# Kernel tuning notes

Measured on AMD Instinct MI355X. Metric: run time of the kernel, lower is better.

The kernel has to match this reference:

```python
import jax, jax.numpy as jnp
import numpy as np

# Static config (mirrors FBPinn __init__ args)
NW = 16            # nwindows (1D case)
D0, D1 = 0.0, 100.0  # domain
OVERLAP = 0.25
SIGMA = 0.5
HIDDEN = 3         # number of hidden layers in each subdomain NN
NEURONS = 64
U_MEAN, U_SD = 0.0, 1.0
N = 100_000        # number of collocation points


def _geometry():
    """partition_domain + get_midpoints + get_midpoints_overlap (1D)."""
    width = (D1 - D0) / NW
    i = np.arange(NW)
    lo = np.where(i == 0, D0, D0 + (i - OVERLAP / 2) * width)
    hi = np.where(i == NW - 1, D1, D0 + (i + 1 + OVERLAP / 2) * width)
    means = (lo + hi) / 2
    std = (hi - lo) / 2
    ovm = np.empty(NW + 1)
    ovm[0] = lo[0]
    ovm[NW] = hi[-1]
    ovm[1:NW] = (hi[:-1] + lo[1:]) / 2  # midpoint of each overlap region
    f32 = lambda a: jnp.asarray(a, jnp.float32)
    return f32(lo), f32(hi), f32(means), f32(std), f32(ovm)


def setup_inputs() -> dict:
    key = jax.random.key(0)
    ks = jax.random.split(key, 7)
    x = jax.random.uniform(ks[0], (N,), jnp.float32, minval=D0, maxval=D1)
    s_in = 1.0  # fan_in = 1
    s_h = 1.0 / np.sqrt(NEURONS)
    return {
        "x": x,
        "W_in": jax.random.normal(ks[1], (NW, NEURONS), jnp.float32) * s_in,
        "b_in": jax.random.normal(ks[2], (NW, NEURONS), jnp.float32) * 0.1,
        "W_h": jax.random.normal(ks[3], (HIDDEN - 1, NW, NEURONS, NEURONS), jnp.float32) * s_h,
        "b_h": jax.random.normal(ks[4], (HIDDEN - 1, NW, NEURONS), jnp.float32) * 0.1,
        "W_out": jax.random.normal(ks[5], (NW, NEURONS), jnp.float32) * s_h,
        "b_out": jax.random.normal(ks[6], (NW,), jnp.float32) * 0.1,
    }


def reference(x, W_in, b_in, W_h, b_h, W_out, b_out):
    lo, hi, means, std, ovm = _geometry()
    # Normalize inputs per subdomain: [W, N]
    xn = (x[None, :] - means[:, None]) / std[:, None]
    # Batched per-window MLP (tanh), one fused pass over all windows.
    h = jnp.tanh(xn[:, :, None] * W_in[:, None, :] + b_in[:, None, :])  # [W, N, H]
    for l in range(HIDDEN - 1):
        h = jnp.tanh(jnp.einsum("wni,wio->wno", h, W_h[l]) + b_h[l][:, None, :])
    out = jnp.einsum("wni,wi->wn", h, W_out) + b_out[:, None]  # [W, N]
    out = out * U_SD + U_MEAN
    # Sigmoid window functions (compute_window, 1D): [W, N]
    win = jax.nn.sigmoid((x[None, :] - ovm[:-1, None]) / SIGMA) * \
          jax.nn.sigmoid(-(x[None, :] - ovm[1:, None]) / SIGMA)
    # Strict in-subdomain mask, as in forward(): (lo < x) & (x < hi)
    mask = (lo[:, None] < x[None, :]) & (x[None, :] < hi[:, None])
    pred = jnp.sum(jnp.where(mask, win * out, jnp.float32(0.0)), axis=0)  # [N]
    return pred
```

## Files before the change

kernel.cpp:

```cpp
#include <hip/hip_runtime.h>


#define NW    16
#define NEUR  64
#define BLK   256
#define CAP   10240
#define CSTR  16
#define GX    64
#define DSFENCE() asm volatile("" ::: "memory")

typedef _Float16 v8h __attribute__((ext_vector_type(8)));
typedef float    v4f __attribute__((ext_vector_type(4)));
typedef _Float16 h2  __attribute__((ext_vector_type(2)));
typedef unsigned v4u __attribute__((ext_vector_type(4)));

__device__ __forceinline__ float fast_tanh(float x) {
    float e = __expf(x + x);
    return 1.0f - 2.0f * __builtin_amdgcn_rcpf(e + 1.0f);
}
__device__ __forceinline__ float fast_sigmoid(float z) {
    return __builtin_amdgcn_rcpf(1.0f + __expf(-z));
}
__device__ __forceinline__ v8h zero8() {
    v8h z;
    #pragma unroll
    for (int j = 0; j < 8; ++j) z[j] = (_Float16)0.0f;
    return z;
}

__global__ __launch_bounds__(1024) void pass1_bucket(
    const float* __restrict__ x, int n,
    int* __restrict__ cnt, int* __restrict__ list,
    float* __restrict__ out) {
    __shared__ int lcnt[NW];
    __shared__ int lbase[NW];
    const int tid = threadIdx.x;
    if (tid < NW) lcnt[tid] = 0;
    __syncthreads();

    const int i = blockIdx.x * 1024 + tid;
    int w0 = -1, w1 = -1, p0 = 0, p1 = 0;
    if (i < n) {
        out[i] = 0.0f;
        float xv = x[i];
        #pragma unroll
        for (int w = 0; w < NW; ++w) {
            float lo = (w == 0)      ? 0.0f   : ((float)w - 0.125f) * 6.25f;
            float hi = (w == NW - 1) ? 100.0f : ((float)w + 1.125f) * 6.25f;
            if (lo < xv && xv < hi) {
                if (w0 < 0) w0 = w; else w1 = w;
            }
        }
        if (w0 >= 0) p0 = atomicAdd(&lcnt[w0], 1);
        if (w1 >= 0) p1 = atomicAdd(&lcnt[w1], 1);
    }
    __syncthreads();
    if (tid < NW)
        lbase[tid] = atomicAdd(&cnt[tid * CSTR], lcnt[tid]);
    __syncthreads();

    if (w0 >= 0) { int p = lbase[w0] + p0; if (p < CAP) list[w0 * CAP + p] = i; }
    if (w1 >= 0) { int p = lbase[w1] + p1; if (p < CAP) list[w1 * CAP + p] = i; }
}

__global__ __launch_bounds__(256) void pass2_mlp(
    const float* __restrict__ x,
    const float* __restrict__ W_in, const float* __restrict__ b_in,
    const float* __restrict__ W_h,  const float* __restrict__ b_h,
    const float* __restrict__ W_out, const float* __restrict__ b_out,
    const int* __restrict__ cnt, const int* __restrict__ list,
    float* __restrict__ out, int npts) {
    __shared__ _Float16 aH[16 * 512];
    __shared__ _Float16 aIn[4 * 512];
    __shared__ _Float16 aOut[2 * 512];
    __shared__ float    biasH[128];
    __shared__ unsigned Hp[4 * 1024];

    const int tid = threadIdx.x;
    const int w   = blockIdx.y;
    const int count = min(cnt[w * CSTR], GX * 128);
    if (blockIdx.x * 128 >= count) return;

    const int lane = tid & 63;
    const int wid  = tid >> 6;
    const int n16  = lane & 15;
    const int quad = lane >> 4;

    #pragma unroll
    for (int p = 0; p < 4; ++p) {
        int f  = wid * 4 + p;
        int l  = f >> 3, mt = (f >> 1) & 3, ks = f & 1;
        const float* Ws = W_h + (l * NW + w) * 4096;
        int m  = mt * 16 + n16;
        int k0 = ks * 32 + quad * 8;
        v8h a;
        #pragma unroll
        for (int j = 0; j < 8; ++j)
            a[j] = (_Float16)Ws[(k0 + j) * 64 + m];
        *(v8h*)(&aH[f * 512 + lane * 8]) = a;
    }
    {
        int mt = wid, m = mt * 16 + n16;
        v8h a = zero8();
        if (quad == 0) {
            a[0] = (_Float16)W_in[w * 64 + m];
            a[1] = (_Float16)b_in[w * 64 + m];
        }
        *(v8h*)(&aIn[mt * 512 + lane * 8]) = a;
    }
    if (wid < 2) {
        int ks = wid;
        v8h a = zero8();
        if (n16 == 0) {
            int k0 = ks * 32 + quad * 8;
            #pragma unroll
            for (int j = 0; j < 8; ++j)
                a[j] = (_Float16)W_out[w * 64 + k0 + j];
        }
        *(v8h*)(&aOut[ks * 512 + lane * 8]) = a;
    }
    if (tid < 128)
        biasH[tid] = b_h[((tid >> 6) * NW + w) * 64 + (tid & 63)];
    __syncthreads();

    float lo = (w == 0)      ? 0.0f   : ((float)w - 0.125f) * 6.25f;
    float hi = (w == NW - 1) ? 100.0f : ((float)w + 1.125f) * 6.25f;
    float mean    = 0.5f * (lo + hi);
    float inv_std = 1.0f / (0.5f * (hi - lo));
    float ow0 = (float)w * 6.25f;
    float ow1 = (float)(w + 1) * 6.25f;
    float bo  = b_out[w];

    float xv[2], xn[2];
    bool  act[2];
    int   idx[2];
    #pragma unroll
    for (int t = 0; t < 2; ++t) {
        int kpt = blockIdx.x * 128 + wid * 32 + t * 16 + n16;
        act[t]  = (kpt < count) && (lane < 16);
        int kk  = (kpt < count) ? kpt : 0;
        int id  = list[w * CAP + kk];
        if ((unsigned)id >= (unsigned)npts) id = 0;
        idx[t] = id;
        xv[t]  = x[id];
        xn[t]  = (xv[t] - mean) * inv_std;
    }

    unsigned* HpW = Hp + wid * 1024;

    {
        v8h b[2];
        #pragma unroll
        for (int t = 0; t < 2; ++t) {
            b[t] = zero8();
            if (quad == 0) { b[t][0] = (_Float16)xn[t]; b[t][1] = (_Float16)1.0f; }
        }
        #pragma unroll
        for (int mt = 0; mt < 4; ++mt) {
            v8h a = *(const v8h*)(&aIn[mt * 512 + lane * 8]);
            #pragma unroll
            for (int t = 0; t < 2; ++t) {
                v4f c = {0.0f, 0.0f, 0.0f, 0.0f};
                c = __builtin_amdgcn_mfma_f32_16x16x32_f16(a, b[t], c, 0, 0, 0);
                int k2 = mt * 8 + quad * 2;
                h2 q0, q1;
                q0[0] = (_Float16)fast_tanh(c[0]);
                q0[1] = (_Float16)fast_tanh(c[1]);
                q1[0] = (_Float16)fast_tanh(c[2]);
                q1[1] = (_Float16)fast_tanh(c[3]);
                HpW[t * 512 + k2 * 16 + n16]       = __builtin_bit_cast(unsigned, q0);
                HpW[t * 512 + (k2 + 1) * 16 + n16] = __builtin_bit_cast(unsigned, q1);
            }
        }
    }
    DSFENCE();

    #pragma unroll
    for (int l = 0; l < 2; ++l) {
        v4f d[2][4];
        #pragma unroll
        for (int t = 0; t < 2; ++t)
            #pragma unroll
            for (int mt = 0; mt < 4; ++mt)
                d[t][mt] = (v4f){0.0f, 0.0f, 0.0f, 0.0f};
        #pragma unroll
        for (int ks = 0; ks < 2; ++ks) {
            v8h b[2];
            #pragma unroll
            for (int t = 0; t < 2; ++t) {
                v4u bw;
                #pragma unroll
                for (int j2 = 0; j2 < 4; ++j2)
                    bw[j2] = HpW[t * 512 + (ks * 16 + quad * 4 + j2) * 16 + n16];
                b[t] = __builtin_bit_cast(v8h, bw);
            }
            #pragma unroll
            for (int mt = 0; mt < 4; ++mt) {
                v8h a = *(const v8h*)(&aH[(l * 8 + mt * 2 + ks) * 512 + lane * 8]);
                #pragma unroll
                for (int t = 0; t < 2; ++t)
                    d[t][mt] = __builtin_amdgcn_mfma_f32_16x16x32_f16(
                                   a, b[t], d[t][mt], 0, 0, 0);
            }
        }
        DSFENCE();
        const float* bl = biasH + l * 64;
        #pragma unroll
        for (int t = 0; t < 2; ++t) {
            #pragma unroll
            for (int mt = 0; mt < 4; ++mt) {
                int m0 = mt * 16 + quad * 4;
                int k2 = m0 >> 1;
                h2 q0, q1;
                q0[0] = (_Float16)fast_tanh(d[t][mt][0] + bl[m0]);
                q0[1] = (_Float16)fast_tanh(d[t][mt][1] + bl[m0 + 1]);
                q1[0] = (_Float16)fast_tanh(d[t][mt][2] + bl[m0 + 2]);
                q1[1] = (_Float16)fast_tanh(d[t][mt][3] + bl[m0 + 3]);
                HpW[t * 512 + k2 * 16 + n16]       = __builtin_bit_cast(unsigned, q0);
                HpW[t * 512 + (k2 + 1) * 16 + n16] = __builtin_bit_cast(unsigned, q1);
            }
        }
        DSFENCE();
    }

    {
        v4f e[2] = {{0.0f,0.0f,0.0f,0.0f}, {0.0f,0.0f,0.0f,0.0f}};
        #pragma unroll
        for (int ks = 0; ks < 2; ++ks) {
            v8h a = *(const v8h*)(&aOut[ks * 512 + lane * 8]);
            #pragma unroll
            for (int t = 0; t < 2; ++t) {
                v4u bw;
                #pragma unroll
                for (int j2 = 0; j2 < 4; ++j2)
                    bw[j2] = HpW[t * 512 + (ks * 16 + quad * 4 + j2) * 16 + n16];
                v8h b = __builtin_bit_cast(v8h, bw);
                e[t] = __builtin_amdgcn_mfma_f32_16x16x32_f16(a, b, e[t], 0, 0, 0);
            }
        }
        #pragma unroll
        for (int t = 0; t < 2; ++t) {
            float outv = e[t][0] + bo;
            float win = fast_sigmoid((xv[t] - ow0) * 2.0f) *
                        fast_sigmoid((ow1 - xv[t]) * 2.0f);
            if (act[t]) atomicAdd(&out[idx[t]], win * outv);
        }
    }
}

extern "C" void kernel_launch(void* const* d_in, const int* in_sizes, int n_in,
                              void* d_out, int out_size, void* d_ws, size_t ws_size,
                              hipStream_t stream) {
    const float* x     = (const float*)d_in[0];
    const float* W_in  = (const float*)d_in[1];
    const float* b_in  = (const float*)d_in[2];
    const float* W_h   = (const float*)d_in[3];
    const float* b_h   = (const float*)d_in[4];
    const float* W_out = (const float*)d_in[5];
    const float* b_out = (const float*)d_in[6];
    float* out = (float*)d_out;
    const int n = in_sizes[0];

    int* cnt  = (int*)d_ws;
    int* list = (int*)((char*)d_ws + 1024);

    hipMemsetAsync(cnt, 0, NW * CSTR * sizeof(int), stream);

    pass1_bucket<<<(n + 1023) / 1024, 1024, 0, stream>>>(x, n, cnt, list, out);

    dim3 grid(GX, NW);
    pass2_mlp<<<grid, BLK, 0, stream>>>(x, W_in, b_in, W_h, b_h, W_out, b_out,
                                        cnt, list, out, n);
}
```

Before: 85.66 us.

## Fuse bucketing into MLP kernel with per-block shared-memory point lists

Replaces the global bucketing pass and its workspace list with a single kernel. Each (segment, window) block scans its 1/64 slice of x, collects in-window points into a shared-memory index list, then loops over them in 128-point tiles through the MFMA MLP. Output zeroing moves to a memset. This removes one kernel launch, the global atomics and the list round-trip through global memory. In exchange, every block reads its whole x segment for all 16 windows, and LCAP=1600 relies on the uniform input distribution to avoid overflowing the shared list.

```diff
diff --git a/kernel.cpp b/kernel.cpp
--- a/kernel.cpp
+++ b/kernel.cpp
@@ -4,9 +4,8 @@
 #define NW    16
 #define NEUR  64
 #define BLK   256
-#define CAP   10240
-#define CSTR  16
-#define GX    64
+#define NSEG  64
+#define LCAP  1600
 #define DSFENCE() asm volatile("" ::: "memory")
 
 typedef _Float16 v8h __attribute__((ext_vector_type(8)));
@@ -28,63 +27,45 @@
     return z;
 }
 
-__global__ __launch_bounds__(1024) void pass1_bucket(
-    const float* __restrict__ x, int n,
-    int* __restrict__ cnt, int* __restrict__ list,
-    float* __restrict__ out) {
-    __shared__ int lcnt[NW];
-    __shared__ int lbase[NW];
-    const int tid = threadIdx.x;
-    if (tid < NW) lcnt[tid] = 0;
-    __syncthreads();
-
-    const int i = blockIdx.x * 1024 + tid;
-    int w0 = -1, w1 = -1, p0 = 0, p1 = 0;
-    if (i < n) {
-        out[i] = 0.0f;
-        float xv = x[i];
-        #pragma unroll
-        for (int w = 0; w < NW; ++w) {
-            float lo = (w == 0)      ? 0.0f   : ((float)w - 0.125f) * 6.25f;
-            float hi = (w == NW - 1) ? 100.0f : ((float)w + 1.125f) * 6.25f;
-            if (lo < xv && xv < hi) {
-                if (w0 < 0) w0 = w; else w1 = w;
-            }
-        }
-        if (w0 >= 0) p0 = atomicAdd(&lcnt[w0], 1);
-        if (w1 >= 0) p1 = atomicAdd(&lcnt[w1], 1);
-    }
-    __syncthreads();
-    if (tid < NW)
-        lbase[tid] = atomicAdd(&cnt[tid * CSTR], lcnt[tid]);
-    __syncthreads();
-
-    if (w0 >= 0) { int p = lbase[w0] + p0; if (p < CAP) list[w0 * CAP + p] = i; }
-    if (w1 >= 0) { int p = lbase[w1] + p1; if (p < CAP) list[w1 * CAP + p] = i; }
-}
-
-__global__ __launch_bounds__(256) void pass2_mlp(
+__global__ __launch_bounds__(256, 3) void fused_fbpinn(
     const float* __restrict__ x,
     const float* __restrict__ W_in, const float* __restrict__ b_in,
     const float* __restrict__ W_h,  const float* __restrict__ b_h,
     const float* __restrict__ W_out, const float* __restrict__ b_out,
-    const int* __restrict__ cnt, const int* __restrict__ list,
-    float* __restrict__ out, int npts) {
+    float* __restrict__ out, int n) {
     __shared__ _Float16 aH[16 * 512];
     __shared__ _Float16 aIn[4 * 512];
     __shared__ _Float16 aOut[2 * 512];
     __shared__ float    biasH[128];
     __shared__ unsigned Hp[4 * 1024];
-
-    const int tid = threadIdx.x;
-    const int w   = blockIdx.y;
-    const int count = min(cnt[w * CSTR], GX * 128);
-    if (blockIdx.x * 128 >= count) return;
-
+    __shared__ int      lidx[LCAP];
+    __shared__ int      scnt;
+
+    const int tid  = threadIdx.x;
+    const int seg  = blockIdx.x;
+    const int w    = blockIdx.y;
     const int lane = tid & 63;
     const int wid  = tid >> 6;
     const int n16  = lane & 15;
     const int quad = lane >> 4;
+
+    float lo = (w == 0)      ? 0.0f   : ((float)w - 0.125f) * 6.25f;
+    float hi = (w == NW - 1) ? 100.0f : ((float)w + 1.125f) * 6.25f;
+
+    if (tid == 0) scnt = 0;
+    __syncthreads();
+    {
+        const int chunk = (n + NSEG - 1) / NSEG;
+        const int i0 = seg * chunk;
+        const int i1 = min(n, i0 + chunk);
+        for (int i = i0 + tid; i < i1; i += BLK) {
+            float xv = x[i];
+            if (lo < xv && xv < hi) {
+                int p = atomicAdd(&scnt, 1);
+                lidx[p] = i;
+            }
+        }
+    }
 
     #pragma unroll
     for (int p = 0; p < 4; ++p) {
@@ -123,128 +104,131 @@
         biasH[tid] = b_h[((tid >> 6) * NW + w) * 64 + (tid & 63)];
     __syncthreads();
 
-    float lo = (w == 0)      ? 0.0f   : ((float)w - 0.125f) * 6.25f;
-    float hi = (w == NW - 1) ? 100.0f : ((float)w + 1.125f) * 6.25f;
+    const int m_cnt = scnt;
+    if (m_cnt == 0) return;
+
     float mean    = 0.5f * (lo + hi);
     float inv_std = 1.0f / (0.5f * (hi - lo));
     float ow0 = (float)w * 6.25f;
     float ow1 = (float)(w + 1) * 6.25f;
     float bo  = b_out[w];
 
-    float xv[2], xn[2];
-    bool  act[2];
-    int   idx[2];
-    #pragma unroll
-    for (int t = 0; t < 2; ++t) {
-        int kpt = blockIdx.x * 128 + wid * 32 + t * 16 + n16;
-        act[t]  = (kpt < count) && (lane < 16);
-        int kk  = (kpt < count) ? kpt : 0;
-        int id  = list[w * CAP + kk];
-        if ((unsigned)id >= (unsigned)npts) id = 0;
-        idx[t] = id;
-        xv[t]  = x[id];
-        xn[t]  = (xv[t] - mean) * inv_std;
-    }
-
     unsigned* HpW = Hp + wid * 1024;
 
-    {
-        v8h b[2];
+    for (int base = 0; base < m_cnt; base += 128) {
+        float xv[2], xn[2];
+        bool  act[2];
+        int   idx[2];
         #pragma unroll
         for (int t = 0; t < 2; ++t) {
-            b[t] = zero8();
-            if (quad == 0) { b[t][0] = (_Float16)xn[t]; b[t][1] = (_Float16)1.0f; }
-        }
+            int kpt = base + wid * 32 + t * 16 + n16;
+            act[t]  = (kpt < m_cnt) && (lane < 16);
+            int kk  = (kpt < m_cnt) ? kpt : 0;
+            int id  = lidx[kk];
+            idx[t] = id;
+            xv[t]  = x[id];
+            xn[t]  = (xv[t] - mean) * inv_std;
+        }
+
+        {
+            v8h b[2];
+            #pragma unroll
+            for (int t = 0; t < 2; ++t) {
+                b[t] = zero8();
+                if (quad == 0) { b[t][0] = (_Float16)xn[t]; b[t][1] = (_Float16)1.0f; }
+            }
+            #pragma unroll
+            for (int mt = 0; mt < 4; ++mt) {
+                v8h a = *(const v8h*)(&aIn[mt * 512 + lane * 8]);
+                #pragma unroll
+                for (int t = 0; t < 2; ++t) {
+                    v4f c = {0.0f, 0.0f, 0.0f, 0.0f};
+                    c = __builtin_amdgcn_mfma_f32_16x16x32_f16(a, b[t], c, 0, 0, 0);
+                    int k2 = mt * 8 + quad * 2;
+                    h2 q0, q1;
+                    q0[0] = (_Float16)fast_tanh(c[0]);
+                    q0[1] = (_Float16)fast_tanh(c[1]);
+                    q1[0] = (_Float16)fast_tanh(c[2]);
+                    q1[1] = (_Float16)fast_tanh(c[3]);
+                    HpW[t * 512 + k2 * 16 + n16]       = __builtin_bit_cast(unsigned, q0);
+                    HpW[t * 512 + (k2 + 1) * 16 + n16] = __builtin_bit_cast(unsigned, q1);
+                }
+            }
+        }
+        DSFENCE();
+
         #pragma unroll
-        for (int mt = 0; mt < 4; ++mt) {
-            v8h a = *(const v8h*)(&aIn[mt * 512 + lane * 8]);
+        for (int l = 0; l < 2; ++l) {
+            v4f d[2][4];
+            #pragma unroll
+            for (int t = 0; t < 2; ++t)
+                #pragma unroll
+                for (int mt = 0; mt < 4; ++mt)
+                    d[t][mt] = (v4f){0.0f, 0.0f, 0.0f, 0.0f};
+            #pragma unroll
+            for (int ks = 0; ks < 2; ++ks) {
+                v8h b[2];
+                #pragma unroll
+                for (int t = 0; t < 2; ++t) {
+                    v4u bw;
+                    #pragma unroll
+                    for (int j2 = 0; j2 < 4; ++j2)
+                        bw[j2] = HpW[t * 512 + (ks * 16 + quad * 4 + j2) * 16 + n16];
+                    b[t] = __builtin_bit_cast(v8h, bw);
+                }
+                #pragma unroll
+                for (int mt = 0; mt < 4; ++mt) {
+                    v8h a = *(const v8h*)(&aH[(l * 8 + mt * 2 + ks) * 512 + lane * 8]);
+                    #pragma unroll
+                    for (int t = 0; t < 2; ++t)
+                        d[t][mt] = __builtin_amdgcn_mfma_f32_16x16x32_f16(
+                                       a, b[t], d[t][mt], 0, 0, 0);
+                }
+            }
+            DSFENCE();
+            const float* bl = biasH + l * 64;
             #pragma unroll
             for (int t = 0; t < 2; ++t) {
-                v4f c = {0.0f, 0.0f, 0.0f, 0.0f};
-                c = __builtin_amdgcn_mfma_f32_16x16x32_f16(a, b[t], c, 0, 0, 0);
-                int k2 = mt * 8 + quad * 2;
-                h2 q0, q1;
-                q0[0] = (_Float16)fast_tanh(c[0]);
-                q0[1] = (_Float16)fast_tanh(c[1]);
-                q1[0] = (_Float16)fast_tanh(c[2]);
-                q1[1] = (_Float16)fast_tanh(c[3]);
-                HpW[t * 512 + k2 * 16 + n16]       = __builtin_bit_cast(unsigned, q0);
-                HpW[t * 512 + (k2 + 1) * 16 + n16] = __builtin_bit_cast(unsigned, q1);
-            }
-        }
-    }
-    DSFENCE();
-
-    #pragma unroll
-    for (int l = 0; l < 2; ++l) {
-        v4f d[2][4];
-        #pragma unroll
-        for (int t = 0; t < 2; ++t)
-            #pragma unroll
-            for (int mt = 0; mt < 4; ++mt)
-                d[t][mt] = (v4f){0.0f, 0.0f, 0.0f, 0.0f};
-        #pragma unroll
-        for (int ks = 0; ks < 2; ++ks) {
-            v8h b[2];
+                #pragma unroll
+                for (int mt = 0; mt < 4; ++mt) {
+                    int m0 = mt * 16 + quad * 4;
+                    int k2 = m0 >> 1;
+                    h2 q0, q1;
+                    q0[0] = (_Float16)fast_tanh(d[t][mt][0] + bl[m0]);
+                    q0[1] = (_Float16)fast_tanh(d[t][mt][1] + bl[m0 + 1]);
+                    q1[0] = (_Float16)fast_tanh(d[t][mt][2] + bl[m0 + 2]);
+                    q1[1] = (_Float16)fast_tanh(d[t][mt][3] + bl[m0 + 3]);
+                    HpW[t * 512 + k2 * 16 + n16]       = __builtin_bit_cast(unsigned, q0);
+                    HpW[t * 512 + (k2 + 1) * 16 + n16] = __builtin_bit_cast(unsigned, q1);
+                }
+            }
+            DSFENCE();
+        }
+
+        {
+            v4f e[2] = {{0.0f,0.0f,0.0f,0.0f}, {0.0f,0.0f,0.0f,0.0f}};
+            #pragma unroll
+            for (int ks = 0; ks < 2; ++ks) {
+                v8h a = *(const v8h*)(&aOut[ks * 512 + lane * 8]);
+                #pragma unroll
+                for (int t = 0; t < 2; ++t) {
+                    v4u bw;
+                    #pragma unroll
+                    for (int j2 = 0; j2 < 4; ++j2)
+                        bw[j2] = HpW[t * 512 + (ks * 16 + quad * 4 + j2) * 16 + n16];
+                    v8h b = __builtin_bit_cast(v8h, bw);
+                    e[t] = __builtin_amdgcn_mfma_f32_16x16x32_f16(a, b, e[t], 0, 0, 0);
+                }
+            }
             #pragma unroll
             for (int t = 0; t < 2; ++t) {
-                v4u bw;
-                #pragma unroll
-                for (int j2 = 0; j2 < 4; ++j2)
-                    bw[j2] = HpW[t * 512 + (ks * 16 + quad * 4 + j2) * 16 + n16];
-                b[t] = __builtin_bit_cast(v8h, bw);
-            }
-            #pragma unroll
-            for (int mt = 0; mt < 4; ++mt) {
-                v8h a = *(const v8h*)(&aH[(l * 8 + mt * 2 + ks) * 512 + lane * 8]);
-                #pragma unroll
-                for (int t = 0; t < 2; ++t)
-                    d[t][mt] = __builtin_amdgcn_mfma_f32_16x16x32_f16(
-                                   a, b[t], d[t][mt], 0, 0, 0);
+                float outv = e[t][0] + bo;
+                float win = fast_sigmoid((xv[t] - ow0) * 2.0f) *
+                            fast_sigmoid((ow1 - xv[t]) * 2.0f);
+                if (act[t]) atomicAdd(&out[idx[t]], win * outv);
             }
         }
         DSFENCE();
-        const float* bl = biasH + l * 64;
-        #pragma unroll
-        for (int t = 0; t < 2; ++t) {
-            #pragma unroll
-            for (int mt = 0; mt < 4; ++mt) {
-                int m0 = mt * 16 + quad * 4;
-                int k2 = m0 >> 1;
-                h2 q0, q1;
-                q0[0] = (_Float16)fast_tanh(d[t][mt][0] + bl[m0]);
-                q0[1] = (_Float16)fast_tanh(d[t][mt][1] + bl[m0 + 1]);
-                q1[0] = (_Float16)fast_tanh(d[t][mt][2] + bl[m0 + 2]);
-                q1[1] = (_Float16)fast_tanh(d[t][mt][3] + bl[m0 + 3]);
-                HpW[t * 512 + k2 * 16 + n16]       = __builtin_bit_cast(unsigned, q0);
-                HpW[t * 512 + (k2 + 1) * 16 + n16] = __builtin_bit_cast(unsigned, q1);
-            }
-        }
-        DSFENCE();
-    }
-
-    {
-        v4f e[2] = {{0.0f,0.0f,0.0f,0.0f}, {0.0f,0.0f,0.0f,0.0f}};
-        #pragma unroll
-        for (int ks = 0; ks < 2; ++ks) {
-            v8h a = *(const v8h*)(&aOut[ks * 512 + lane * 8]);
-            #pragma unroll
-            for (int t = 0; t < 2; ++t) {
-                v4u bw;
-                #pragma unroll
-                for (int j2 = 0; j2 < 4; ++j2)
-                    bw[j2] = HpW[t * 512 + (ks * 16 + quad * 4 + j2) * 16 + n16];
-                v8h b = __builtin_bit_cast(v8h, bw);
-                e[t] = __builtin_amdgcn_mfma_f32_16x16x32_f16(a, b, e[t], 0, 0, 0);
-            }
-        }
-        #pragma unroll
-        for (int t = 0; t < 2; ++t) {
-            float outv = e[t][0] + bo;
-            float win = fast_sigmoid((xv[t] - ow0) * 2.0f) *
-                        fast_sigmoid((ow1 - xv[t]) * 2.0f);
-            if (act[t]) atomicAdd(&out[idx[t]], win * outv);
-        }
     }
 }
 
@@ -261,14 +245,9 @@
     float* out = (float*)d_out;
     const int n = in_sizes[0];
 
-    int* cnt  = (int*)d_ws;
-    int* list = (int*)((char*)d_ws + 1024);
-
-    hipMemsetAsync(cnt, 0, NW * CSTR * sizeof(int), stream);
-
-    pass1_bucket<<<(n + 1023) / 1024, 1024, 0, stream>>>(x, n, cnt, list, out);
-
-    dim3 grid(GX, NW);
-    pass2_mlp<<<grid, BLK, 0, stream>>>(x, W_in, b_in, W_h, b_h, W_out, b_out,
-                                        cnt, list, out, n);
-}
+    hipMemsetAsync(out, 0, (size_t)n * sizeof(float), stream);
+
+    dim3 grid(NSEG, NW);
+    fused_fbpinn<<<grid, BLK, 0, stream>>>(x, W_in, b_in, W_h, b_h,
+                                           W_out, b_out, out, n);
+}
```

New measurement: 87.84 us. 1.03x slower.
